# Performance work log

Measured on AMD Instinct MI355X. Metric: run time of the kernel, lower is better.

## Reference

```python
import jax, jax.numpy as jnp
import numpy as np

L, B, E, H = 512, 4, 512, 8
D = E // H  # head_dim = 64


def setup_inputs() -> dict:
    key = jax.random.key(0)
    ks = jax.random.split(key, 7)
    query = jax.random.normal(ks[0], (L, B, E), dtype=jnp.float32)
    relation_k = jax.random.normal(ks[1], (B, L, L, D), dtype=jnp.float32)
    relation_v = jax.random.normal(ks[2], (B, L, L, D), dtype=jnp.float32)
    # xavier-uniform-ish scale for the fused QKV projection
    lim = float(np.sqrt(6.0 / (3 * E + E)))
    in_proj_weight = jax.random.uniform(ks[3], (3 * E, E), jnp.float32, -lim, lim)
    in_proj_bias = jnp.zeros((3 * E,), jnp.float32)
    lim_o = float(np.sqrt(1.0 / E))
    out_proj_weight = jax.random.uniform(ks[4], (E, E), jnp.float32, -lim_o, lim_o)
    out_proj_bias = jnp.zeros((E,), jnp.float32)
    return {
        "query": query,
        "relation_k": relation_k,
        "relation_v": relation_v,
        "in_proj_weight": in_proj_weight,
        "in_proj_bias": in_proj_bias,
        "out_proj_weight": out_proj_weight,
        "out_proj_bias": out_proj_bias,
    }


def reference(query, relation_k, relation_v, in_proj_weight, in_proj_bias,
              out_proj_weight, out_proj_bias):
    # query == key == value (qkv_same path), shape (L, B, E)
    scaling = float(D) ** -0.5
    qkv = query @ in_proj_weight.T + in_proj_bias          # (L, B, 3E)
    q, k, v = jnp.split(qkv, 3, axis=-1)                   # each (L, B, E)
    q = q * scaling

    def to_bhld(t):  # (L, B, E) -> (B, H, L, D)
        return t.reshape(L, B, H, D).transpose(1, 2, 0, 3)

    q, k, v = to_bhld(q), to_bhld(k), to_bhld(v)

    # content scores
    scores = jnp.einsum('bhid,bhjd->bhij', q, k)           # (B, H, L, L)

    # relation_k term: torch does a flat .view of (B*H, L, L, D) -> (B*H*L, D, L)
    # which is a row-major REINTERPRETATION (not a transpose). Replicate via reshape:
    rk = relation_k.reshape(B, L, D, L)                    # per-(b,i) block (L*D,) -> (D, L)
    scores = scores + jnp.einsum('bhid,bidj->bhij', q, rk)

    w = jax.nn.softmax(scores, axis=-1)
    w = jnp.where(jnp.isnan(w), jnp.zeros_like(w), w)      # NaN guard as in original

    out = jnp.einsum('bhij,bhjd->bhid', w, v)              # (B, H, L, D)
    # relation_v term: (B*H*L, 1, L) @ (B*H*L, L, D) -> per-query weighted relation values
    out = out + jnp.einsum('bhij,bijd->bhid', w, relation_v)

    out = out.transpose(2, 0, 1, 3).reshape(L, B, E)       # (B,H,L,D) -> (L,B,E)
    return out @ out_proj_weight.T + out_proj_bias
```

## Files before the change

### kernel.cpp

```cpp
#include <hip/hip_runtime.h>
#include <stdint.h>


typedef short short8 __attribute__((ext_vector_type(8)));
typedef float f32x4 __attribute__((ext_vector_type(4)));

static __device__ __forceinline__ uint16_t f2bf(float f) {
  uint32_t u = __float_as_uint(f);
  uint32_t r = (u + 0x7FFFu + ((u >> 16) & 1u)) >> 16;
  return (uint16_t)r;
}
static __device__ __forceinline__ float bf2f(uint16_t h) {
  return __uint_as_float(((uint32_t)h) << 16);
}
static __device__ __forceinline__ short8 ld8(const uint16_t* p) {
  return *(const short8*)p;
}
#define MFMA(a, b, c) __builtin_amdgcn_mfma_f32_16x16x32_bf16((a), (b), (c), 0, 0, 0)

__global__ void k_conv(const float* __restrict__ in, uint16_t* __restrict__ hi,
                       uint16_t* __restrict__ lo, int n) {
  int i = blockIdx.x * blockDim.x + threadIdx.x;
  int stride = gridDim.x * blockDim.x;
  for (; i < n; i += stride) {
    float f = in[i];
    uint16_t h = f2bf(f);
    hi[i] = h;
    if (lo) lo[i] = f2bf(f - bf2f(h));
  }
}

__global__ __launch_bounds__(256) void k_inproj(
    const uint16_t* __restrict__ a_hi, const uint16_t* __restrict__ a_lo,
    const uint16_t* __restrict__ w_hi, const uint16_t* __restrict__ w_lo,
    const float* __restrict__ bias, float* __restrict__ q_s,
    uint16_t* __restrict__ q_bf, uint16_t* __restrict__ k_bf,
    uint16_t* __restrict__ v_bf) {
  const int wave = threadIdx.x >> 6, lane = threadIdx.x & 63;
  const int wr = wave >> 1, wc = wave & 1;
  const int rif = lane & 15, kg = lane >> 4;
  const int rbase = blockIdx.x * 64 + wr * 32;
  const int cbase = blockIdx.y * 64 + wc * 32;
  f32x4 acc[2][2] = {};
  for (int ks = 0; ks < 512; ks += 32) {
    int kofs = ks + kg * 8;
    short8 aH[2], aL[2], bH[2], bL[2];
#pragma unroll
    for (int m = 0; m < 2; ++m) {
      size_t idx = (size_t)(rbase + m * 16 + rif) * 512 + kofs;
      aH[m] = ld8(a_hi + idx);
      aL[m] = ld8(a_lo + idx);
    }
#pragma unroll
    for (int n = 0; n < 2; ++n) {
      size_t idx = (size_t)(cbase + n * 16 + rif) * 512 + kofs;
      bH[n] = ld8(w_hi + idx);
      bL[n] = ld8(w_lo + idx);
    }
#pragma unroll
    for (int m = 0; m < 2; ++m)
#pragma unroll
      for (int n = 0; n < 2; ++n) {
        acc[m][n] = MFMA(aH[m], bH[n], acc[m][n]);
        acc[m][n] = MFMA(aH[m], bL[n], acc[m][n]);
        acc[m][n] = MFMA(aL[m], bH[n], acc[m][n]);
      }
  }
#pragma unroll
  for (int m = 0; m < 2; ++m)
#pragma unroll
    for (int n = 0; n < 2; ++n)
#pragma unroll
      for (int r = 0; r < 4; ++r) {
        int row = rbase + m * 16 + kg * 4 + r;
        int col = cbase + n * 16 + rif;
        float val = acc[m][n][r] + bias[col];
        int l = row >> 2, b = row & 3;
        int sel = col >> 9, h = (col >> 6) & 7, d = col & 63;
        size_t oidx = ((size_t)(b * 8 + h) * 512 + l) * 64 + d;
        if (sel == 0) {
          val *= 0.125f;
          q_s[oidx] = val;
          q_bf[oidx] = f2bf(val);
        } else if (sel == 1) {
          k_bf[oidx] = f2bf(val);
        } else {
          v_bf[oidx] = f2bf(val);
        }
      }
}

__global__ __launch_bounds__(256) void k_vtrans(const uint16_t* __restrict__ v_bf,
                                                uint16_t* __restrict__ v_t) {
  __shared__ uint16_t tile[512 * 64];
  const size_t base = (size_t)blockIdx.x * 512 * 64;
  const uint4* s4 = (const uint4*)(v_bf + base);
  uint4* t4 = (uint4*)tile;
#pragma unroll
  for (int it = 0; it < 16; ++it) t4[it * 256 + threadIdx.x] = s4[it * 256 + threadIdx.x];
  __syncthreads();
  uint16_t* dst = v_t + base;
  int d = threadIdx.x >> 2, jb = (threadIdx.x & 3) * 128;
  for (int c = 0; c < 16; ++c) {
    int j0 = jb + c * 8;
    uint16_t tmp[8];
#pragma unroll
    for (int e = 0; e < 8; ++e) tmp[e] = tile[(j0 + e) * 64 + d];
    *(uint4*)(dst + (size_t)d * 512 + j0) = *(uint4*)tmp;
  }
}

__global__ __launch_bounds__(256) void k_scores(const uint16_t* __restrict__ q_bf,
                                                const uint16_t* __restrict__ k_bf,
                                                float* __restrict__ scores) {
  const int bh = blockIdx.x;
  const uint16_t* qb = q_bf + (size_t)bh * 512 * 64;
  const uint16_t* kb = k_bf + (size_t)bh * 512 * 64;
  const int wave = threadIdx.x >> 6, lane = threadIdx.x & 63;
  const int wr = wave >> 1, wc = wave & 1;
  const int rif = lane & 15, kg = lane >> 4;
  const int ibase = blockIdx.y * 64 + wr * 32;
  const int jbase = blockIdx.z * 64 + wc * 32;
  f32x4 acc[2][2] = {};
#pragma unroll
  for (int ks = 0; ks < 64; ks += 32) {
    int kofs = ks + kg * 8;
    short8 A[2], Bb[2];
#pragma unroll
    for (int m = 0; m < 2; ++m) A[m] = ld8(qb + (size_t)(ibase + m * 16 + rif) * 64 + kofs);
#pragma unroll
    for (int n = 0; n < 2; ++n) Bb[n] = ld8(kb + (size_t)(jbase + n * 16 + rif) * 64 + kofs);
#pragma unroll
    for (int m = 0; m < 2; ++m)
#pragma unroll
      for (int n = 0; n < 2; ++n) acc[m][n] = MFMA(A[m], Bb[n], acc[m][n]);
  }
  float* sc = scores + (size_t)bh * 512 * 512;
#pragma unroll
  for (int m = 0; m < 2; ++m)
#pragma unroll
    for (int n = 0; n < 2; ++n)
#pragma unroll
      for (int r = 0; r < 4; ++r)
        sc[(size_t)(ibase + m * 16 + kg * 4 + r) * 512 + (jbase + n * 16 + rif)] = acc[m][n][r];
}

__global__ __launch_bounds__(256) void k_rksoftmax(
    const float* __restrict__ relation_k, const float* __restrict__ q_s,
    const float* __restrict__ scores, uint16_t* __restrict__ w_bf) {
  __shared__ float qv[64 * 8];
  __shared__ float sx[8 * 512];
  const int b = blockIdx.x >> 9, i = blockIdx.x & 511;
  const int t = threadIdx.x;
  for (int e = t; e < 512; e += 256) {
    int h = e >> 6, d = e & 63;
    qv[d * 8 + h] = q_s[(((size_t)b * 8 + h) * 512 + i) * 64 + d];
  }
  __syncthreads();
  const int quad = t & 127, rep = t >> 7;
  const int j0 = quad * 4;
  const float* rkb = relation_k + ((size_t)b * 512 + i) * 32768;
  f32x4 acc[8] = {};
  for (int dd = 0; dd < 32; ++dd) {
    int d = rep * 32 + dd;
    f32x4 rk4 = *(const f32x4*)(rkb + (size_t)d * 512 + j0);
    f32x4 q0 = *(const f32x4*)&qv[d * 8];
    f32x4 q1 = *(const f32x4*)&qv[d * 8 + 4];
#pragma unroll
    for (int h = 0; h < 4; ++h)
#pragma unroll
      for (int c = 0; c < 4; ++c) acc[h][c] += q0[h] * rk4[c];
#pragma unroll
    for (int h = 0; h < 4; ++h)
#pragma unroll
      for (int c = 0; c < 4; ++c) acc[4 + h][c] += q1[h] * rk4[c];
  }
  if (rep == 1) {
#pragma unroll
    for (int h = 0; h < 8; ++h) *(f32x4*)&sx[h * 512 + j0] = acc[h];
  }
  __syncthreads();
  if (rep == 0) {
#pragma unroll
    for (int h = 0; h < 8; ++h) {
      f32x4 o = *(f32x4*)&sx[h * 512 + j0];
#pragma unroll
      for (int c = 0; c < 4; ++c) o[c] += acc[h][c];
      *(f32x4*)&sx[h * 512 + j0] = o;
    }
  }
  __syncthreads();
  const int wave = t >> 6, lane = t & 63;
  for (int hh = 0; hh < 2; ++hh) {
    int h = wave * 2 + hh;
    const float* srow = scores + (((size_t)b * 8 + h) * 512 + i) * 512;
    float s[8], m = -1e30f;
#pragma unroll
    for (int jj = 0; jj < 8; ++jj) {
      int j = jj * 64 + lane;
      s[jj] = srow[j] + sx[h * 512 + j];
      m = fmaxf(m, s[jj]);
    }
    for (int o = 32; o > 0; o >>= 1) m = fmaxf(m, __shfl_xor(m, o));
    float e[8], sum = 0.f;
#pragma unroll
    for (int jj = 0; jj < 8; ++jj) {
      e[jj] = __expf(s[jj] - m);
      sum += e[jj];
    }
    for (int o = 32; o > 0; o >>= 1) sum += __shfl_xor(sum, o);
    float r = 1.f / sum;
    uint16_t* wrow = w_bf + (((size_t)b * 8 + h) * 512 + i) * 512;
#pragma unroll
    for (int jj = 0; jj < 8; ++jj) wrow[jj * 64 + lane] = f2bf(e[jj] * r);
  }
}

__global__ __launch_bounds__(256) void k_pv(const uint16_t* __restrict__ w_bf,
                                            const uint16_t* __restrict__ v_t,
                                            float* __restrict__ attn) {
  const int bh = blockIdx.x;
  const uint16_t* wb = w_bf + (size_t)bh * 512 * 512;
  const uint16_t* vt = v_t + (size_t)bh * 64 * 512;
  const int wave = threadIdx.x >> 6, lane = threadIdx.x & 63;
  const int wr = wave >> 1, wc = wave & 1;
  const int rif = lane & 15, kg = lane >> 4;
  const int ibase = blockIdx.y * 64 + wr * 32;
  const int dbase = wc * 32;
  f32x4 acc[2][2] = {};
  for (int ks = 0; ks < 512; ks += 32) {
    int kofs = ks + kg * 8;
    short8 A[2], Bb[2];
#pragma unroll
    for (int m = 0; m < 2; ++m) A[m] = ld8(wb + (size_t)(ibase + m * 16 + rif) * 512 + kofs);
#pragma unroll
    for (int n = 0; n < 2; ++n) Bb[n] = ld8(vt + (size_t)(dbase + n * 16 + rif) * 512 + kofs);
#pragma unroll
    for (int m = 0; m < 2; ++m)
#pragma unroll
      for (int n = 0; n < 2; ++n) acc[m][n] = MFMA(A[m], Bb[n], acc[m][n]);
  }
#pragma unroll
  for (int m = 0; m < 2; ++m)
#pragma unroll
    for (int n = 0; n < 2; ++n)
#pragma unroll
      for (int r = 0; r < 4; ++r)
        attn[((size_t)bh * 512 + ibase + m * 16 + kg * 4 + r) * 64 + (dbase + n * 16 + rif)] =
            acc[m][n][r];
}

__global__ __launch_bounds__(256) void k_rv(const float* __restrict__ relation_v,
                                            const uint16_t* __restrict__ w_bf,
                                            const float* __restrict__ attn,
                                            uint16_t* __restrict__ attn_bf) {
  __shared__ float wT[512 * 8];
  __shared__ float partials[4 * 8 * 64];
  const int b = blockIdx.x >> 9, i = blockIdx.x & 511;
  const int t = threadIdx.x;
  {
    int h = t >> 5, jb = (t & 31) * 16;
    const uint16_t* wrow = w_bf + (((size_t)b * 8 + h) * 512 + i) * 512 + jb;
    uint16_t tmp[16];
    *(uint4*)tmp = *(const uint4*)wrow;
    *(uint4*)(tmp + 8) = *(const uint4*)(wrow + 8);
#pragma unroll
    for (int m = 0; m < 16; ++m) wT[(jb + m) * 8 + h] = bf2f(tmp[m]);
  }
  __syncthreads();
  const int wave = t >> 6, lane = t & 63;
  const float* rvb = relation_v + ((size_t)b * 512 + i) * 32768;
  float acc[8] = {};
  for (int jj = 0; jj < 128; ++jj) {
    int j = wave * 128 + jj;
    float rv = rvb[(size_t)j * 64 + lane];
    f32x4 w0 = *(const f32x4*)&wT[j * 8];
    f32x4 w1 = *(const f32x4*)&wT[j * 8 + 4];
#pragma unroll
    for (int h = 0; h < 4; ++h) acc[h] += w0[h] * rv;
#pragma unroll
    for (int h = 0; h < 4; ++h) acc[4 + h] += w1[h] * rv;
  }
#pragma unroll
  for (int h = 0; h < 8; ++h) partials[(wave * 8 + h) * 64 + lane] = acc[h];
  __syncthreads();
  for (int e = t; e < 512; e += 256) {
    int h = e >> 6, d = e & 63;
    float s = attn[(((size_t)b * 8 + h) * 512 + i) * 64 + d];
#pragma unroll
    for (int ww = 0; ww < 4; ++ww) s += partials[(ww * 8 + h) * 64 + d];
    attn_bf[((size_t)i * 4 + b) * 512 + h * 64 + d] = f2bf(s);
  }
}

__global__ __launch_bounds__(256) void k_outproj(const uint16_t* __restrict__ attn_bf,
                                                 const uint16_t* __restrict__ wo_bf,
                                                 const float* __restrict__ bias,
                                                 float* __restrict__ out) {
  const int wave = threadIdx.x >> 6, lane = threadIdx.x & 63;
  const int wr = wave >> 1, wc = wave & 1;
  const int rif = lane & 15, kg = lane >> 4;
  const int rbase = blockIdx.x * 64 + wr * 32;
  const int cbase = blockIdx.y * 64 + wc * 32;
  f32x4 acc[2][2] = {};
  for (int ks = 0; ks < 512; ks += 32) {
    int kofs = ks + kg * 8;
    short8 A[2], Bb[2];
#pragma unroll
    for (int m = 0; m < 2; ++m) A[m] = ld8(attn_bf + (size_t)(rbase + m * 16 + rif) * 512 + kofs);
#pragma unroll
    for (int n = 0; n < 2; ++n) Bb[n] = ld8(wo_bf + (size_t)(cbase + n * 16 + rif) * 512 + kofs);
#pragma unroll
    for (int m = 0; m < 2; ++m)
#pragma unroll
      for (int n = 0; n < 2; ++n) acc[m][n] = MFMA(A[m], Bb[n], acc[m][n]);
  }
#pragma unroll
  for (int m = 0; m < 2; ++m)
#pragma unroll
    for (int n = 0; n < 2; ++n)
#pragma unroll
      for (int r = 0; r < 4; ++r) {
        int row = rbase + m * 16 + kg * 4 + r;
        int col = cbase + n * 16 + rif;
        out[(size_t)row * 512 + col] = acc[m][n][r] + bias[col];
      }
}

extern "C" void kernel_launch(void* const* d_in, const int* in_sizes, int n_in,
                              void* d_out, int out_size, void* d_ws, size_t ws_size,
                              hipStream_t stream) {
  const float* query = (const float*)d_in[0];
  const float* relation_k = (const float*)d_in[1];
  const float* relation_v = (const float*)d_in[2];
  const float* in_w = (const float*)d_in[3];
  const float* in_b = (const float*)d_in[4];
  const float* out_w = (const float*)d_in[5];
  const float* out_b = (const float*)d_in[6];
  float* out = (float*)d_out;
  char* ws = (char*)d_ws;

  uint16_t* a_hi  = (uint16_t*)(ws + 0);
  uint16_t* a_lo  = (uint16_t*)(ws + 2097152);
  uint16_t* w_hi  = (uint16_t*)(ws + 4194304);
  uint16_t* w_lo  = (uint16_t*)(ws + 5767168);
  uint16_t* wo_bf = (uint16_t*)(ws + 7340032);
  float*    q_s   = (float*)   (ws + 7864320);
  uint16_t* q_bf  = (uint16_t*)(ws + 12058624);
  uint16_t* k_bf  = (uint16_t*)(ws + 14155776);
  uint16_t* v_bf  = (uint16_t*)(ws + 16252928);
  uint16_t* v_t   = (uint16_t*)(ws + 18350080);
  float*    attn  = (float*)   (ws + 20447232);
  uint16_t* attn_bf = (uint16_t*)(ws + 24641536);
  uint16_t* wprob = (uint16_t*)(ws + 26738688);
  float*    scores = (float*)  (ws + 43515904);

  k_conv<<<dim3(768), 256, 0, stream>>>(in_w, w_hi, w_lo, 1536 * 512);
  k_conv<<<dim3(1024), 256, 0, stream>>>(query, a_hi, a_lo, 2048 * 512);
  k_conv<<<dim3(256), 256, 0, stream>>>(out_w, wo_bf, (uint16_t*)nullptr, 512 * 512);
  k_inproj<<<dim3(32, 24), 256, 0, stream>>>(a_hi, a_lo, w_hi, w_lo, in_b, q_s, q_bf, k_bf, v_bf);
  k_vtrans<<<dim3(32), 256, 0, stream>>>(v_bf, v_t);
  k_scores<<<dim3(32, 8, 8), 256, 0, stream>>>(q_bf, k_bf, scores);
  k_rksoftmax<<<dim3(2048), 256, 0, stream>>>(relation_k, q_s, scores, wprob);
  k_pv<<<dim3(32, 8), 256, 0, stream>>>(wprob, v_t, attn);
  k_rv<<<dim3(2048), 256, 0, stream>>>(relation_v, wprob, attn, attn_bf);
  k_outproj<<<dim3(32, 8), 256, 0, stream>>>(attn_bf, wo_bf, out_b, out);
}
```

Measured before the change: 222.8 us.

## Fuse relation-value matmul into softmax kernel and drop V transpose

```diff
diff --git a/kernel.cpp b/kernel.cpp
--- a/kernel.cpp
+++ b/kernel.cpp
@@ -1,9 +1,11 @@
 #include <hip/hip_runtime.h>
+#include <hip/hip_fp16.h>
 #include <stdint.h>
 
 
 typedef short short8 __attribute__((ext_vector_type(8)));
 typedef float f32x4 __attribute__((ext_vector_type(4)));
+typedef unsigned short u16x4 __attribute__((ext_vector_type(4)));
 
 static __device__ __forceinline__ uint16_t f2bf(float f) {
   uint32_t u = __float_as_uint(f);
@@ -18,15 +20,40 @@
 }
 #define MFMA(a, b, c) __builtin_amdgcn_mfma_f32_16x16x32_bf16((a), (b), (c), 0, 0, 0)
 
-__global__ void k_conv(const float* __restrict__ in, uint16_t* __restrict__ hi,
-                       uint16_t* __restrict__ lo, int n) {
-  int i = blockIdx.x * blockDim.x + threadIdx.x;
-  int stride = gridDim.x * blockDim.x;
-  for (; i < n; i += stride) {
-    float f = in[i];
-    uint16_t h = f2bf(f);
-    hi[i] = h;
-    if (lo) lo[i] = f2bf(f - bf2f(h));
+__global__ __launch_bounds__(256) void k_conv_all(
+    const float* __restrict__ in_w, const float* __restrict__ query,
+    const float* __restrict__ out_w, uint16_t* __restrict__ w_hi,
+    uint16_t* __restrict__ w_lo, uint16_t* __restrict__ a_hi,
+    uint16_t* __restrict__ a_lo, uint16_t* __restrict__ wo_bf) {
+  int e = (blockIdx.x * 256 + threadIdx.x) * 4;
+  if (e < 786432) {
+    f32x4 v = *(const f32x4*)(in_w + e);
+    u16x4 hi, lo;
+#pragma unroll
+    for (int k = 0; k < 4; ++k) {
+      hi[k] = f2bf(v[k]);
+      lo[k] = f2bf(v[k] - bf2f(hi[k]));
+    }
+    *(u16x4*)(w_hi + e) = hi;
+    *(u16x4*)(w_lo + e) = lo;
+  } else if (e < 786432 + 1048576) {
+    int o = e - 786432;
+    f32x4 v = *(const f32x4*)(query + o);
+    u16x4 hi, lo;
+#pragma unroll
+    for (int k = 0; k < 4; ++k) {
+      hi[k] = f2bf(v[k]);
+      lo[k] = f2bf(v[k] - bf2f(hi[k]));
+    }
+    *(u16x4*)(a_hi + o) = hi;
+    *(u16x4*)(a_lo + o) = lo;
+  } else {
+    int o = e - 1835008;
+    f32x4 v = *(const f32x4*)(out_w + o);
+    u16x4 hi;
+#pragma unroll
+    for (int k = 0; k < 4; ++k) hi[k] = f2bf(v[k]);
+    *(u16x4*)(wo_bf + o) = hi;
   }
 }
 
@@ -90,29 +117,9 @@
       }
 }
 
-__global__ __launch_bounds__(256) void k_vtrans(const uint16_t* __restrict__ v_bf,
-                                                uint16_t* __restrict__ v_t) {
-  __shared__ uint16_t tile[512 * 64];
-  const size_t base = (size_t)blockIdx.x * 512 * 64;
-  const uint4* s4 = (const uint4*)(v_bf + base);
-  uint4* t4 = (uint4*)tile;
-#pragma unroll
-  for (int it = 0; it < 16; ++it) t4[it * 256 + threadIdx.x] = s4[it * 256 + threadIdx.x];
-  __syncthreads();
-  uint16_t* dst = v_t + base;
-  int d = threadIdx.x >> 2, jb = (threadIdx.x & 3) * 128;
-  for (int c = 0; c < 16; ++c) {
-    int j0 = jb + c * 8;
-    uint16_t tmp[8];
-#pragma unroll
-    for (int e = 0; e < 8; ++e) tmp[e] = tile[(j0 + e) * 64 + d];
-    *(uint4*)(dst + (size_t)d * 512 + j0) = *(uint4*)tmp;
-  }
-}
-
 __global__ __launch_bounds__(256) void k_scores(const uint16_t* __restrict__ q_bf,
                                                 const uint16_t* __restrict__ k_bf,
-                                                float* __restrict__ scores) {
+                                                __half* __restrict__ scores) {
   const int bh = blockIdx.x;
   const uint16_t* qb = q_bf + (size_t)bh * 512 * 64;
   const uint16_t* kb = k_bf + (size_t)bh * 512 * 64;
@@ -135,23 +142,27 @@
 #pragma unroll
       for (int n = 0; n < 2; ++n) acc[m][n] = MFMA(A[m], Bb[n], acc[m][n]);
   }
-  float* sc = scores + (size_t)bh * 512 * 512;
+  __half* sc = scores + (size_t)bh * 512 * 512;
 #pragma unroll
   for (int m = 0; m < 2; ++m)
 #pragma unroll
     for (int n = 0; n < 2; ++n)
 #pragma unroll
       for (int r = 0; r < 4; ++r)
-        sc[(size_t)(ibase + m * 16 + kg * 4 + r) * 512 + (jbase + n * 16 + rif)] = acc[m][n][r];
-}
-
-__global__ __launch_bounds__(256) void k_rksoftmax(
-    const float* __restrict__ relation_k, const float* __restrict__ q_s,
-    const float* __restrict__ scores, uint16_t* __restrict__ w_bf) {
+        sc[(size_t)(ibase + m * 16 + kg * 4 + r) * 512 + (jbase + n * 16 + rif)] =
+            __float2half(acc[m][n][r]);
+}
+
+__global__ __launch_bounds__(256) void k_mega(
+    const float* __restrict__ relation_k, const float* __restrict__ relation_v,
+    const float* __restrict__ q_s, const __half* __restrict__ scores,
+    uint16_t* __restrict__ wprob, uint16_t* __restrict__ rv_bf) {
   __shared__ float qv[64 * 8];
   __shared__ float sx[8 * 512];
+  __shared__ uint16_t wlds[8 * 512];
   const int b = blockIdx.x >> 9, i = blockIdx.x & 511;
   const int t = threadIdx.x;
+  const int wave = t >> 6, lane = t & 63;
   for (int e = t; e < 512; e += 256) {
     int h = e >> 6, d = e & 63;
     qv[d * 8 + h] = q_s[(((size_t)b * 8 + h) * 512 + i) * 64 + d];
@@ -160,68 +171,102 @@
   const int quad = t & 127, rep = t >> 7;
   const int j0 = quad * 4;
   const float* rkb = relation_k + ((size_t)b * 512 + i) * 32768;
-  f32x4 acc[8] = {};
-  for (int dd = 0; dd < 32; ++dd) {
-    int d = rep * 32 + dd;
-    f32x4 rk4 = *(const f32x4*)(rkb + (size_t)d * 512 + j0);
-    f32x4 q0 = *(const f32x4*)&qv[d * 8];
-    f32x4 q1 = *(const f32x4*)&qv[d * 8 + 4];
-#pragma unroll
-    for (int h = 0; h < 4; ++h)
-#pragma unroll
-      for (int c = 0; c < 4; ++c) acc[h][c] += q0[h] * rk4[c];
-#pragma unroll
-    for (int h = 0; h < 4; ++h)
-#pragma unroll
-      for (int c = 0; c < 4; ++c) acc[4 + h][c] += q1[h] * rk4[c];
-  }
-  if (rep == 1) {
-#pragma unroll
-    for (int h = 0; h < 8; ++h) *(f32x4*)&sx[h * 512 + j0] = acc[h];
+  {
+    f32x4 acc[8] = {};
+    for (int dd = 0; dd < 32; ++dd) {
+      int d = rep * 32 + dd;
+      f32x4 rk4 = *(const f32x4*)(rkb + (size_t)d * 512 + j0);
+      f32x4 q0 = *(const f32x4*)&qv[d * 8];
+      f32x4 q1 = *(const f32x4*)&qv[d * 8 + 4];
+#pragma unroll
+      for (int h = 0; h < 4; ++h)
+#pragma unroll
+        for (int c = 0; c < 4; ++c) acc[h][c] += q0[h] * rk4[c];
+#pragma unroll
+      for (int h = 0; h < 4; ++h)
+#pragma unroll
+        for (int c = 0; c < 4; ++c) acc[4 + h][c] += q1[h] * rk4[c];
+    }
+    if (rep == 1) {
+#pragma unroll
+      for (int h = 0; h < 8; ++h) *(f32x4*)&sx[h * 512 + j0] = acc[h];
+    }
+    __syncthreads();
+    if (rep == 0) {
+#pragma unroll
+      for (int h = 0; h < 8; ++h) {
+        f32x4 o = *(f32x4*)&sx[h * 512 + j0];
+#pragma unroll
+        for (int c = 0; c < 4; ++c) o[c] += acc[h][c];
+        *(f32x4*)&sx[h * 512 + j0] = o;
+      }
+    }
   }
   __syncthreads();
-  if (rep == 0) {
-#pragma unroll
-    for (int h = 0; h < 8; ++h) {
-      f32x4 o = *(f32x4*)&sx[h * 512 + j0];
-#pragma unroll
-      for (int c = 0; c < 4; ++c) o[c] += acc[h][c];
-      *(f32x4*)&sx[h * 512 + j0] = o;
-    }
-  }
-  __syncthreads();
-  const int wave = t >> 6, lane = t & 63;
   for (int hh = 0; hh < 2; ++hh) {
     int h = wave * 2 + hh;
-    const float* srow = scores + (((size_t)b * 8 + h) * 512 + i) * 512;
+    const __half* srow = scores + (((size_t)b * 8 + h) * 512 + i) * 512;
     float s[8], m = -1e30f;
 #pragma unroll
     for (int jj = 0; jj < 8; ++jj) {
       int j = jj * 64 + lane;
-      s[jj] = srow[j] + sx[h * 512 + j];
+      s[jj] = __half2float(srow[j]) + sx[h * 512 + j];
       m = fmaxf(m, s[jj]);
     }
     for (int o = 32; o > 0; o >>= 1) m = fmaxf(m, __shfl_xor(m, o));
-    float e[8], sum = 0.f;
+    float ex[8], sum = 0.f;
 #pragma unroll
     for (int jj = 0; jj < 8; ++jj) {
-      e[jj] = __expf(s[jj] - m);
-      sum += e[jj];
+      ex[jj] = __expf(s[jj] - m);
+      sum += ex[jj];
     }
     for (int o = 32; o > 0; o >>= 1) sum += __shfl_xor(sum, o);
     float r = 1.f / sum;
-    uint16_t* wrow = w_bf + (((size_t)b * 8 + h) * 512 + i) * 512;
-#pragma unroll
-    for (int jj = 0; jj < 8; ++jj) wrow[jj * 64 + lane] = f2bf(e[jj] * r);
+    uint16_t* wrow = wprob + (((size_t)b * 8 + h) * 512 + i) * 512;
+#pragma unroll
+    for (int jj = 0; jj < 8; ++jj) {
+      int j = jj * 64 + lane;
+      uint16_t wv = f2bf(ex[jj] * r);
+      wrow[j] = wv;
+      int ba = (h * 1024 + j * 2) ^ ((h & 7) << 4);
+      *(uint16_t*)((char*)wlds + ba) = wv;
+    }
+  }
+  __syncthreads();
+  const int rif = lane & 15, kg = lane >> 4;
+  const int dt = wave;
+  const float* rvb = relation_v + ((size_t)b * 512 + i) * 32768;
+  f32x4 acc2 = {};
+  for (int ks = 0; ks < 16; ++ks) {
+    short8 A = {};
+    if (rif < 8) {
+      int ba = (rif * 1024 + (ks * 32 + kg * 8) * 2) ^ ((rif & 7) << 4);
+      A = *(const short8*)((const char*)wlds + ba);
+    }
+    uint16_t tb[8];
+#pragma unroll
+    for (int e = 0; e < 8; ++e)
+      tb[e] = f2bf(rvb[(size_t)(ks * 32 + kg * 8 + e) * 64 + dt * 16 + rif]);
+    short8 Bb = *(const short8*)tb;
+    acc2 = MFMA(A, Bb, acc2);
+  }
+  if (kg < 2) {
+#pragma unroll
+    for (int r = 0; r < 4; ++r) {
+      int h = kg * 4 + r;
+      int d = dt * 16 + rif;
+      rv_bf[((size_t)i * 4 + b) * 512 + h * 64 + d] = f2bf(acc2[r]);
+    }
   }
 }
 
 __global__ __launch_bounds__(256) void k_pv(const uint16_t* __restrict__ w_bf,
-                                            const uint16_t* __restrict__ v_t,
-                                            float* __restrict__ attn) {
+                                            const uint16_t* __restrict__ v_bf,
+                                            uint16_t* __restrict__ pv_bf) {
   const int bh = blockIdx.x;
+  const int b = bh >> 3, h = bh & 7;
   const uint16_t* wb = w_bf + (size_t)bh * 512 * 512;
-  const uint16_t* vt = v_t + (size_t)bh * 64 * 512;
+  const uint16_t* vb = v_bf + (size_t)bh * 512 * 64;
   const int wave = threadIdx.x >> 6, lane = threadIdx.x & 63;
   const int wr = wave >> 1, wc = wave & 1;
   const int rif = lane & 15, kg = lane >> 4;
@@ -234,7 +279,12 @@
 #pragma unroll
     for (int m = 0; m < 2; ++m) A[m] = ld8(wb + (size_t)(ibase + m * 16 + rif) * 512 + kofs);
 #pragma unroll
-    for (int n = 0; n < 2; ++n) Bb[n] = ld8(vt + (size_t)(dbase + n * 16 + rif) * 512 + kofs);
+    for (int n = 0; n < 2; ++n) {
+      uint16_t tb[8];
+#pragma unroll
+      for (int e = 0; e < 8; ++e) tb[e] = vb[(size_t)(kofs + e) * 64 + dbase + n * 16 + rif];
+      Bb[n] = *(const short8*)tb;
+    }
 #pragma unroll
     for (int m = 0; m < 2; ++m)
 #pragma unroll
@@ -245,55 +295,15 @@
 #pragma unroll
     for (int n = 0; n < 2; ++n)
 #pragma unroll
-      for (int r = 0; r < 4; ++r)
-        attn[((size_t)bh * 512 + ibase + m * 16 + kg * 4 + r) * 64 + (dbase + n * 16 + rif)] =
-            acc[m][n][r];
-}
-
-__global__ __launch_bounds__(256) void k_rv(const float* __restrict__ relation_v,
-                                            const uint16_t* __restrict__ w_bf,
-                                            const float* __restrict__ attn,
-                                            uint16_t* __restrict__ attn_bf) {
-  __shared__ float wT[512 * 8];
-  __shared__ float partials[4 * 8 * 64];
-  const int b = blockIdx.x >> 9, i = blockIdx.x & 511;
-  const int t = threadIdx.x;
-  {
-    int h = t >> 5, jb = (t & 31) * 16;
-    const uint16_t* wrow = w_bf + (((size_t)b * 8 + h) * 512 + i) * 512 + jb;
-    uint16_t tmp[16];
-    *(uint4*)tmp = *(const uint4*)wrow;
-    *(uint4*)(tmp + 8) = *(const uint4*)(wrow + 8);
-#pragma unroll
-    for (int m = 0; m < 16; ++m) wT[(jb + m) * 8 + h] = bf2f(tmp[m]);
-  }
-  __syncthreads();
-  const int wave = t >> 6, lane = t & 63;
-  const float* rvb = relation_v + ((size_t)b * 512 + i) * 32768;
-  float acc[8] = {};
-  for (int jj = 0; jj < 128; ++jj) {
-    int j = wave * 128 + jj;
-    float rv = rvb[(size_t)j * 64 + lane];
-    f32x4 w0 = *(const f32x4*)&wT[j * 8];
-    f32x4 w1 = *(const f32x4*)&wT[j * 8 + 4];
-#pragma unroll
-    for (int h = 0; h < 4; ++h) acc[h] += w0[h] * rv;
-#pragma unroll
-    for (int h = 0; h < 4; ++h) acc[4 + h] += w1[h] * rv;
-  }
-#pragma unroll
-  for (int h = 0; h < 8; ++h) partials[(wave * 8 + h) * 64 + lane] = acc[h];
-  __syncthreads();
-  for (int e = t; e < 512; e += 256) {
-    int h = e >> 6, d = e & 63;
-    float s = attn[(((size_t)b * 8 + h) * 512 + i) * 64 + d];
-#pragma unroll
-    for (int ww = 0; ww < 4; ++ww) s += partials[(ww * 8 + h) * 64 + d];
-    attn_bf[((size_t)i * 4 + b) * 512 + h * 64 + d] = f2bf(s);
-  }
-}
-
-__global__ __launch_bounds__(256) void k_outproj(const uint16_t* __restrict__ attn_bf,
+      for (int r = 0; r < 4; ++r) {
+        int i = ibase + m * 16 + kg * 4 + r;
+        int d = dbase + n * 16 + rif;
+        pv_bf[((size_t)i * 4 + b) * 512 + h * 64 + d] = f2bf(acc[m][n][r]);
+      }
+}
+
+__global__ __launch_bounds__(256) void k_outproj(const uint16_t* __restrict__ rv_a,
+                                                 const uint16_t* __restrict__ pv_a,
                                                  const uint16_t* __restrict__ wo_bf,
                                                  const float* __restrict__ bias,
                                                  float* __restrict__ out) {
@@ -307,7 +317,16 @@
     int kofs = ks + kg * 8;
     short8 A[2], Bb[2];
 #pragma unroll
-    for (int m = 0; m < 2; ++m) A[m] = ld8(attn_bf + (size_t)(rbase + m * 16 + rif) * 512 + kofs);
+    for (int m = 0; m < 2; ++m) {
+      size_t idx = (size_t)(rbase + m * 16 + rif) * 512 + kofs;
+      short8 p = ld8(pv_a + idx);
+      short8 rr = ld8(rv_a + idx);
+      uint16_t tb[8];
+#pragma unroll
+      for (int e = 0; e < 8; ++e)
+        tb[e] = f2bf(bf2f((uint16_t)p[e]) + bf2f((uint16_t)rr[e]));
+      A[m] = *(const short8*)tb;
+    }
 #pragma unroll
     for (int n = 0; n < 2; ++n) Bb[n] = ld8(wo_bf + (size_t)(cbase + n * 16 + rif) * 512 + kofs);
 #pragma unroll
@@ -349,20 +368,15 @@
   uint16_t* q_bf  = (uint16_t*)(ws + 12058624);
   uint16_t* k_bf  = (uint16_t*)(ws + 14155776);
   uint16_t* v_bf  = (uint16_t*)(ws + 16252928);
-  uint16_t* v_t   = (uint16_t*)(ws + 18350080);
-  float*    attn  = (float*)   (ws + 20447232);
-  uint16_t* attn_bf = (uint16_t*)(ws + 24641536);
-  uint16_t* wprob = (uint16_t*)(ws + 26738688);
-  float*    scores = (float*)  (ws + 43515904);
-
-  k_conv<<<dim3(768), 256, 0, stream>>>(in_w, w_hi, w_lo, 1536 * 512);
-  k_conv<<<dim3(1024), 256, 0, stream>>>(query, a_hi, a_lo, 2048 * 512);
-  k_conv<<<dim3(256), 256, 0, stream>>>(out_w, wo_bf, (uint16_t*)nullptr, 512 * 512);
+  uint16_t* rv_bf = (uint16_t*)(ws + 18350080);
+  uint16_t* pv_bf = (uint16_t*)(ws + 20447232);
+  uint16_t* wprob = (uint16_t*)(ws + 22544384);
+  __half*   sc_h  = (__half*)  (ws + 39321600);
+
+  k_conv_all<<<dim3(2048), 256, 0, stream>>>(in_w, query, out_w, w_hi, w_lo, a_hi, a_lo, wo_bf);
   k_inproj<<<dim3(32, 24), 256, 0, stream>>>(a_hi, a_lo, w_hi, w_lo, in_b, q_s, q_bf, k_bf, v_bf);
-  k_vtrans<<<dim3(32), 256, 0, stream>>>(v_bf, v_t);
-  k_scores<<<dim3(32, 8, 8), 256, 0, stream>>>(q_bf, k_bf, scores);
-  k_rksoftmax<<<dim3(2048), 256, 0, stream>>>(relation_k, q_s, scores, wprob);
-  k_pv<<<dim3(32, 8), 256, 0, stream>>>(wprob, v_t, attn);
-  k_rv<<<dim3(2048), 256, 0, stream>>>(relation_v, wprob, attn, attn_bf);
-  k_outproj<<<dim3(32, 8), 256, 0, stream>>>(attn_bf, wo_bf, out_b, out);
-}
+  k_scores<<<dim3(32, 8, 8), 256, 0, stream>>>(q_bf, k_bf, sc_h);
+  k_mega<<<dim3(2048), 256, 0, stream>>>(relation_k, relation_v, q_s, sc_h, wprob, rv_bf);
+  k_pv<<<dim3(32, 8), 256, 0, stream>>>(wprob, v_bf, pv_bf);
+  k_outproj<<<dim3(32, 8), 256, 0, stream>>>(rv_bf, pv_bf, wo_bf, out_b, out);
+}
```

Result: faster. 204.7 us (-8.1%).
